# Optimization experiments

Measured on AMD Instinct MI355X. Metric: run time of the kernel, lower is better.

Reference implementation:

```python
import jax, jax.numpy as jnp
import numpy as np

B, S, H = 2, 2048, 2048
NH, NKV, HD = 16, 4, 128
SCALING = HD ** -0.5


def rotate_half(x):
    x1, x2 = jnp.split(x, 2, axis=-1)
    return jnp.concatenate((-x2, x1), axis=-1)


def apply_rope(t, cos, sin):
    # t: [B, nh, S, HD]; cos/sin: [B, S, HD] -> unsqueeze head dim
    c = cos[:, None, :, :]
    s = sin[:, None, :, :]
    return t * c + rotate_half(t) * s


def setup_inputs() -> dict:
    key = jax.random.key(0)
    k1, k2, k3, k4, k5 = jax.random.split(key, 5)
    hidden_states = jax.random.normal(k1, (B, S, H), dtype=jnp.float32)
    # real RoPE tables
    inv_freq = 1.0 / (10000.0 ** (jnp.arange(0, HD, 2, dtype=jnp.float32) / HD))
    pos = jnp.arange(S, dtype=jnp.float32)
    freqs = jnp.einsum('s,d->sd', pos, inv_freq)              # [S, HD/2]
    emb = jnp.concatenate((freqs, freqs), axis=-1)            # [S, HD]
    cos = jnp.broadcast_to(jnp.cos(emb)[None], (B, S, HD))
    sin = jnp.broadcast_to(jnp.sin(emb)[None], (B, S, HD))
    # additive causal mask [B, 1, S, S]
    causal = jnp.triu(jnp.full((S, S), -1e9, dtype=jnp.float32), k=1)
    attention_mask = jnp.broadcast_to(causal[None, None], (B, 1, S, S))
    sc = 0.02
    wq = jax.random.normal(k2, (NH * HD, H), dtype=jnp.float32) * sc
    wk = jax.random.normal(k3, (NKV * HD, H), dtype=jnp.float32) * sc
    wv = jax.random.normal(k4, (NKV * HD, H), dtype=jnp.float32) * sc
    wo = jax.random.normal(k5, (H, NH * HD), dtype=jnp.float32) * sc
    return {"hidden_states": hidden_states, "cos": cos, "sin": sin,
            "attention_mask": attention_mask, "wq": wq, "wk": wk, "wv": wv, "wo": wo}


def reference(hidden_states, cos, sin, attention_mask, wq, wk, wv, wo):
    x = hidden_states
    # fused-style QKV projections (nn.Linear: x @ W.T), split heads -> [B, nh, S, HD]
    q = (x @ wq.T).reshape(B, S, NH, HD).transpose(0, 2, 1, 3)
    k = (x @ wk.T).reshape(B, S, NKV, HD).transpose(0, 2, 1, 3)
    v = (x @ wv.T).reshape(B, S, NKV, HD).transpose(0, 2, 1, 3)
    q = apply_rope(q, cos, sin)
    k = apply_rope(k, cos, sin)
    # GQA: repeat KV heads (repeat_kv)
    n_rep = NH // NKV
    k = jnp.repeat(k, n_rep, axis=1)
    v = jnp.repeat(v, n_rep, axis=1)
    scores = jnp.einsum('bhqd,bhkd->bhqk', q, k) * SCALING + attention_mask
    attn = jax.nn.softmax(scores.astype(jnp.float32), axis=-1).astype(q.dtype)
    out = jnp.einsum('bhqk,bhkd->bhqd', attn, v)
    out = out.transpose(0, 2, 1, 3).reshape(B, S, NH * HD)
    out = out @ wo.T
    return (out, attn)
```

## Files before the change

### kernel.cpp

```cpp
#include <hip/hip_runtime.h>
#include <cstdint>
#include <cstddef>

typedef __bf16 bf16;
typedef __attribute__((ext_vector_type(8))) __bf16 bf16x8;
typedef __attribute__((ext_vector_type(4))) __bf16 bf16x4;
typedef __attribute__((ext_vector_type(4))) float f32x4;

constexpr int B_ = 2, S_ = 2048, H_ = 2048, NH_ = 16, NKV_ = 4, HD_ = 128;
constexpr float SCALE_ = 0.08838834764831845f;

#define GLDS16(g, l)                                                        \
  __builtin_amdgcn_global_load_lds(                                         \
      (const __attribute__((address_space(1))) void*)(g),                   \
      (__attribute__((address_space(3))) void*)(l), 16, 0, 0)

#define VMCNT0 asm volatile("s_waitcnt vmcnt(0)" ::: "memory")
#define VMCNT4 asm volatile("s_waitcnt vmcnt(4)" ::: "memory")
#define VMCNT8 asm volatile("s_waitcnt vmcnt(8)" ::: "memory")
#define BAR __builtin_amdgcn_s_barrier()

__global__ void cvt_all(const float* __restrict__ hs, const float* __restrict__ wq,
                        const float* __restrict__ wk, const float* __restrict__ wv,
                        const float* __restrict__ wo, bf16* __restrict__ xb,
                        bf16* __restrict__ w3b, bf16* __restrict__ wob) {
  const int stride = gridDim.x * blockDim.x;
  for (int i = blockIdx.x * blockDim.x + threadIdx.x; i < 4718592; i += stride) {
    const float4* s; bf16x4* d; int j;
    if (i < 2097152)      { s = (const float4*)hs; d = (bf16x4*)xb;            j = i; }
    else if (i < 3145728) { s = (const float4*)wq; d = (bf16x4*)w3b;           j = i - 2097152; }
    else if (i < 3407872) { s = (const float4*)wk; d = (bf16x4*)w3b + 1048576; j = i - 3145728; }
    else if (i < 3670016) { s = (const float4*)wv; d = (bf16x4*)w3b + 1310720; j = i - 3407872; }
    else                  { s = (const float4*)wo; d = (bf16x4*)wob;           j = i - 3670016; }
    float4 v = s[j];
    bf16x4 o;
    o[0] = (bf16)v.x; o[1] = (bf16)v.y; o[2] = (bf16)v.z; o[3] = (bf16)v.w;
    d[j] = o;
  }
}

template <int EPI>
__global__ __launch_bounds__(256, 2) void gemm_bt(const bf16* __restrict__ A,
                                                  const bf16* __restrict__ Bm, int K,
                                                  bf16* __restrict__ qb, bf16* __restrict__ kb,
                                                  bf16* __restrict__ vtb, float* __restrict__ Cout) {
  __shared__ __align__(16) bf16 As[2][128 * 64];
  __shared__ __align__(16) bf16 Bs[2][128 * 64];
  const int tid = threadIdx.x;
  const int lane = tid & 63;
  const int wid = tid >> 6;
  const int fid = blockIdx.y * 32 + blockIdx.x;
  const int nwg = gridDim.y * 32;
  const int swz = (fid & 7) * (nwg >> 3) + (fid >> 3);
  const int m0 = (swz & 31) * 128;
  const int n0 = (swz >> 5) * 128;
  const int wm = (wid >> 1) * 64, wn = (wid & 1) * 64;
  const int r = lane & 15, g = lane >> 4;
  f32x4 acc[4][4] = {};

  auto STAGE = [&](int kt, int cc) {
#pragma unroll
    for (int i = 0; i < 4; ++i) {
      int cb = wid * 256 + i * 64;
      int c64 = cb + lane;
      int row = c64 >> 3, cs = (c64 & 7) ^ (row & 7);
      GLDS16(A + (size_t)(m0 + row) * K + kt + cs * 8, &As[cc][cb * 8]);
      GLDS16(Bm + (size_t)(n0 + row) * K + kt + cs * 8, &Bs[cc][cb * 8]);
    }
  };

  STAGE(0, 0);
  int c = 0;
#pragma unroll 1
  for (int kt = 0; kt < K; kt += 64) {
    if (kt + 64 < K) {
      STAGE(kt + 64, c ^ 1);
      VMCNT8;
    } else {
      VMCNT0;
    }
    BAR;
#pragma unroll
    for (int ks = 0; ks < 2; ++ks) {
      bf16x8 af[4], bfr[4];
#pragma unroll
      for (int fm = 0; fm < 4; ++fm)
        af[fm] = *(const bf16x8*)(&As[c][(wm + fm * 16 + r) * 64 + (((ks * 4 + g) ^ (r & 7)) << 3)]);
#pragma unroll
      for (int fn = 0; fn < 4; ++fn)
        bfr[fn] = *(const bf16x8*)(&Bs[c][(wn + fn * 16 + r) * 64 + (((ks * 4 + g) ^ (r & 7)) << 3)]);
#pragma unroll
      for (int fm = 0; fm < 4; ++fm)
#pragma unroll
        for (int fn = 0; fn < 4; ++fn)
          acc[fm][fn] = __builtin_amdgcn_mfma_f32_16x16x32_bf16(af[fm], bfr[fn], acc[fm][fn], 0, 0, 0);
    }
    BAR;
    c ^= 1;
  }

#pragma unroll
  for (int fm = 0; fm < 4; ++fm)
#pragma unroll
    for (int fn = 0; fn < 4; ++fn)
#pragma unroll
      for (int rr = 0; rr < 4; ++rr) {
        int mm = m0 + wm + fm * 16 + g * 4 + rr;
        int nn = n0 + wn + fn * 16 + r;
        float v = acc[fm][fn][rr];
        if (EPI == 1) {
          Cout[(size_t)mm * 2048 + nn] = v;
        } else {
          int b = mm >> 11, s = mm & (S_ - 1);
          int d = nn & 127;
          if (nn < 2048) {
            int hh = nn >> 7;
            qb[(((size_t)b * NH_ + hh) * S_ + s) * HD_ + d] = (bf16)v;
          } else if (nn < 2560) {
            int hh = (nn - 2048) >> 7;
            kb[(((size_t)b * NKV_ + hh) * S_ + s) * HD_ + d] = (bf16)v;
          } else {
            int hh = (nn - 2560) >> 7;
            vtb[(((size_t)b * NKV_ + hh) * HD_ + d) * S_ + s] = (bf16)v;
          }
        }
      }
}

__global__ void rope_kernel(bf16* __restrict__ qb, bf16* __restrict__ kb,
                            const float* __restrict__ cosp, const float* __restrict__ sinp) {
  const int NQ = B_ * NH_ * S_;
  const int NK = B_ * NKV_ * S_;
  const int tot = (NQ + NK) * 8;
  int t = blockIdx.x * blockDim.x + threadIdx.x;
  if (t >= tot) return;
  const int oct = t & 7, rid = t >> 3;
  bf16* base;
  int b, s;
  if (rid < NQ) {
    base = qb + (size_t)rid * HD_;
    s = rid & (S_ - 1);
    b = rid >> 15;
  } else {
    int r2 = rid - NQ;
    base = kb + (size_t)r2 * HD_;
    s = r2 & (S_ - 1);
    b = r2 >> 13;
  }
  const int d = oct * 8;
  const float* cp = cosp + ((size_t)b * S_ + s) * HD_ + d;
  const float* sp = sinp + ((size_t)b * S_ + s) * HD_ + d;
  float4 c0 = *(const float4*)cp, c1 = *(const float4*)(cp + 4);
  float4 s0 = *(const float4*)sp, s1 = *(const float4*)(sp + 4);
  float cc[8] = {c0.x, c0.y, c0.z, c0.w, c1.x, c1.y, c1.z, c1.w};
  float ss[8] = {s0.x, s0.y, s0.z, s0.w, s1.x, s1.y, s1.z, s1.w};
  bf16x8 x1 = *(const bf16x8*)(base + d);
  bf16x8 x2 = *(const bf16x8*)(base + d + 64);
  bf16x8 o1, o2;
#pragma unroll
  for (int i = 0; i < 8; ++i) {
    float a = (float)x1[i], bb = (float)x2[i];
    o1[i] = (bf16)(a * cc[i] - bb * ss[i]);
    o2[i] = (bf16)(bb * cc[i] + a * ss[i]);
  }
  *(bf16x8*)(base + d) = o1;
  *(bf16x8*)(base + d + 64) = o2;
}

__global__ __launch_bounds__(256, 2) void attn_kernel(const bf16* __restrict__ qb,
                                                      const bf16* __restrict__ kb,
                                                      const bf16* __restrict__ vtb,
                                                      bf16* __restrict__ aob,
                                                      float* __restrict__ attn_out) {
  __shared__ __align__(16) bf16 Ks[2][64 * 128];
  __shared__ __align__(16) bf16 Vs[2][128 * 64];
  __shared__ __align__(16) bf16 Ps[64 * 64];
  const int bid = (blockIdx.x & 7) * 64 + (blockIdx.x >> 3);
  const int p = bid & 15;
  const int h = (bid >> 4) & 15;
  const int b = bid >> 8;
  const int kh = h >> 2;
  const int tid = threadIdx.x, lane = tid & 63, wid = tid >> 6;
  const int r = lane & 15, g = lane >> 4;

  const bf16* kbase = kb + ((size_t)b * NKV_ + kh) * S_ * HD_;
  const bf16* vbase = vtb + ((size_t)b * NKV_ + kh) * (size_t)HD_ * S_;
  const size_t ahead = (size_t)(b * NH_ + h) * S_;

  auto stageK = [&](int kt, int cc) {
#pragma unroll
    for (int i = 0; i < 4; ++i) {
      int base = i * 256 + wid * 64;
      int idx = base + lane;
      int row = idx >> 4, ch = (idx & 15) ^ (row & 7);
      GLDS16(kbase + (size_t)(kt * 64 + row) * HD_ + ch * 8, &Ks[cc][base * 8]);
    }
  };
  auto stageV = [&](int kt, int cc) {
#pragma unroll
    for (int i = 0; i < 4; ++i) {
      int base = i * 256 + wid * 64;
      int idx = base + lane;
      int row = idx >> 3, ch = (idx & 7) ^ (row & 7);
      GLDS16(vbase + (size_t)row * S_ + kt * 64 + ch * 8, &Vs[cc][base * 8]);
    }
  };

  int zc = 0;

#pragma unroll 1
  for (int sbi = 0; sbi < 2; ++sbi) {
    const int qt = sbi ? 31 - p : p;
    const int q0 = qt * 64;
    const int nt = qt + 1;
    const bf16* qsrc = qb + ((size_t)(b * NH_ + h) * S_ + q0) * HD_;

    bf16x8 qreg[4];
#pragma unroll
    for (int ks = 0; ks < 4; ++ks)
      qreg[ks] = *(const bf16x8*)(qsrc + (wid * 16 + r) * HD_ + ks * 32 + g * 8);

    float lsum = 0.f;
    stageK(0, 0);
    VMCNT0; BAR;
    int c = 0;
#pragma unroll 1
    for (int kt = 0; kt < nt; ++kt) {
      if (kt + 1 < nt) stageK(kt + 1, c ^ 1);
      const bool dz = (zc <= 30);
      if (dz) {
        int qtz, ktz;
        if (zc < 31 - p) { qtz = p; ktz = p + 1 + zc; }
        else             { qtz = 31 - p; ktz = zc + 1; }
        float* zdst = attn_out + (ahead + qtz * 64) * S_ + ktz * 64;
        float4 z = {0.f, 0.f, 0.f, 0.f};
#pragma unroll
        for (int i = 0; i < 4; ++i) {
          int idx = i * 256 + tid;
          *(float4*)(zdst + (size_t)(idx >> 4) * S_ + (idx & 15) * 4) = z;
        }
        ++zc;
      }
      f32x4 sacc[4] = {};
      __builtin_amdgcn_s_setprio(1);
#pragma unroll
      for (int ks = 0; ks < 4; ++ks)
#pragma unroll
        for (int fn = 0; fn < 4; ++fn) {
          bf16x8 kk = *(const bf16x8*)(&Ks[c][(fn * 16 + r) * 128 + (((ks * 4 + g) ^ (r & 7)) << 3)]);
          sacc[fn] = __builtin_amdgcn_mfma_f32_16x16x32_bf16(kk, qreg[ks], sacc[fn], 0, 0, 0);
        }
      __builtin_amdgcn_s_setprio(0);
      float ts = 0.f;
      if (kt == nt - 1) {
#pragma unroll
        for (int fn = 0; fn < 4; ++fn)
#pragma unroll
          for (int rr = 0; rr < 4; ++rr) {
            bool msk = (fn * 16 + g * 4 + rr) > (wid * 16 + r);
            ts += msk ? 0.f : __expf(sacc[fn][rr] * SCALE_);
          }
      } else {
#pragma unroll
        for (int fn = 0; fn < 4; ++fn)
#pragma unroll
          for (int rr = 0; rr < 4; ++rr) ts += __expf(sacc[fn][rr] * SCALE_);
      }
      ts += __shfl_xor(ts, 16);
      ts += __shfl_xor(ts, 32);
      lsum += ts;
      if (dz) { VMCNT4; } else { VMCNT0; }
      BAR;
      c ^= 1;
    }
    const float rl = 1.0f / lsum;

    f32x4 oacc[8] = {};
    const size_t arow0 = (ahead + q0) * S_;
    stageK(0, 0);
    stageV(0, 0);
    VMCNT0; BAR;
    c = 0;
#pragma unroll 1
    for (int kt = 0; kt < nt; ++kt) {
      if (kt + 1 < nt) { stageK(kt + 1, c ^ 1); stageV(kt + 1, c ^ 1); }
      const int k0 = kt * 64;
      f32x4 sacc[4] = {};
      __builtin_amdgcn_s_setprio(1);
#pragma unroll
      for (int ks = 0; ks < 4; ++ks)
#pragma unroll
        for (int fn = 0; fn < 4; ++fn) {
          bf16x8 kk = *(const bf16x8*)(&Ks[c][(fn * 16 + r) * 128 + (((ks * 4 + g) ^ (r & 7)) << 3)]);
          sacc[fn] = __builtin_amdgcn_mfma_f32_16x16x32_bf16(kk, qreg[ks], sacc[fn], 0, 0, 0);
        }
      __builtin_amdgcn_s_setprio(0);
      const int prow = (wid * 16 + r) * 64;
      if (kt == nt - 1) {
#pragma unroll
        for (int fn = 0; fn < 4; ++fn) {
          bf16x4 pk;
#pragma unroll
          for (int rr = 0; rr < 4; ++rr) {
            bool msk = (fn * 16 + g * 4 + rr) > (wid * 16 + r);
            pk[rr] = (bf16)(msk ? 0.f : __expf(sacc[fn][rr] * SCALE_) * rl);
          }
          *(bf16x4*)(&Ps[prow + ((((fn << 1) | (g >> 1)) ^ (r & 7)) << 3) + ((g & 1) << 2)]) = pk;
        }
      } else {
#pragma unroll
        for (int fn = 0; fn < 4; ++fn) {
          bf16x4 pk;
#pragma unroll
          for (int rr = 0; rr < 4; ++rr)
            pk[rr] = (bf16)(__expf(sacc[fn][rr] * SCALE_) * rl);
          *(bf16x4*)(&Ps[prow + ((((fn << 1) | (g >> 1)) ^ (r & 7)) << 3) + ((g & 1) << 2)]) = pk;
        }
      }
      {
        const int trow = tid >> 2, tcb = (tid & 3) * 16;
        float* dst = attn_out + arow0 + (size_t)trow * S_ + k0 + tcb;
        int ch0 = (tid & 3) * 2;
        bf16x8 p0 = *(const bf16x8*)(&Ps[trow * 64 + ((ch0 ^ (trow & 7)) << 3)]);
        bf16x8 p1 = *(const bf16x8*)(&Ps[trow * 64 + (((ch0 + 1) ^ (trow & 7)) << 3)]);
        float4 o0 = {(float)p0[0], (float)p0[1], (float)p0[2], (float)p0[3]};
        float4 o1 = {(float)p0[4], (float)p0[5], (float)p0[6], (float)p0[7]};
        float4 o2 = {(float)p1[0], (float)p1[1], (float)p1[2], (float)p1[3]};
        float4 o3 = {(float)p1[4], (float)p1[5], (float)p1[6], (float)p1[7]};
        *(float4*)(dst) = o0;
        *(float4*)(dst + 4) = o1;
        *(float4*)(dst + 8) = o2;
        *(float4*)(dst + 12) = o3;
      }
      __builtin_amdgcn_s_setprio(1);
#pragma unroll
      for (int ks = 0; ks < 2; ++ks) {
        bf16x8 pa = *(const bf16x8*)(&Ps[prow + (((ks * 4 + g) ^ (r & 7)) << 3)]);
#pragma unroll
        for (int fn = 0; fn < 8; ++fn) {
          bf16x8 vv = *(const bf16x8*)(&Vs[c][(fn * 16 + r) * 64 + (((ks * 4 + g) ^ (r & 7)) << 3)]);
          oacc[fn] = __builtin_amdgcn_mfma_f32_16x16x32_bf16(pa, vv, oacc[fn], 0, 0, 0);
        }
      }
      __builtin_amdgcn_s_setprio(0);
      VMCNT4; BAR;
      c ^= 1;
    }

#pragma unroll
    for (int fn = 0; fn < 8; ++fn)
#pragma unroll
      for (int rr = 0; rr < 4; ++rr) {
        int q = q0 + wid * 16 + g * 4 + rr;
        aob[((size_t)b * S_ + q) * 2048 + h * HD_ + fn * 16 + r] = (bf16)oacc[fn][rr];
      }
  }
}

extern "C" void kernel_launch(void* const* d_in, const int* in_sizes, int n_in,
                              void* d_out, int out_size, void* d_ws, size_t ws_size,
                              hipStream_t stream) {
  const float* hidden = (const float*)d_in[0];
  const float* cosp = (const float*)d_in[1];
  const float* sinp = (const float*)d_in[2];
  const float* wq = (const float*)d_in[4];
  const float* wk = (const float*)d_in[5];
  const float* wv = (const float*)d_in[6];
  const float* wo = (const float*)d_in[7];
  float* out = (float*)d_out;
  float* attn = out + (size_t)B_ * S_ * H_;

  char* ws = (char*)d_ws;
  bf16* xb  = (bf16*)(ws);
  bf16* w3b = (bf16*)(ws + (16ull << 20));
  bf16* wob = (bf16*)(ws + (28ull << 20));
  bf16* qb  = (bf16*)(ws + (36ull << 20));
  bf16* kb  = (bf16*)(ws + (52ull << 20));
  bf16* vtb = (bf16*)(ws + (56ull << 20));
  bf16* aob = (bf16*)(ws + (60ull << 20));

  cvt_all<<<2048, 256, 0, stream>>>(hidden, wq, wk, wv, wo, xb, w3b, wob);
  gemm_bt<0><<<dim3(32, 24), 256, 0, stream>>>(xb, w3b, 2048, qb, kb, vtb, nullptr);
  rope_kernel<<<2560, 256, 0, stream>>>(qb, kb, cosp, sinp);
  attn_kernel<<<512, 256, 0, stream>>>(qb, kb, vtb, aob, attn);
  gemm_bt<1><<<dim3(32, 16), 256, 0, stream>>>(aob, wob, 2048, nullptr, nullptr, nullptr, out);
}
```

Baseline: 349.7 us.

## Split attention into one q-tile per block, load V to registers, write probs directly

The attention kernel now gives each block a single query tile, in descending order, instead of a balanced pair of tiles. The grid doubles to 1024 blocks and the launch bound rises to 3 blocks per SM. V tiles are read straight from global memory into registers instead of being staged through LDS, which removes the Vs buffers and cuts shared memory use. Probabilities are written to attn_out directly from the fp32 softmax values rather than read back from LDS, and the zeroing of masked tiles is reorganised per block. These changes trade away the original load balancing and add VGPR pressure in exchange for more occupancy and less LDS traffic.

Result: slower. 449.1 us (+28.4%).

```diff
diff --git a/kernel.cpp b/kernel.cpp
--- a/kernel.cpp
+++ b/kernel.cpp
@@ -18,6 +18,7 @@
 #define VMCNT0 asm volatile("s_waitcnt vmcnt(0)" ::: "memory")
 #define VMCNT4 asm volatile("s_waitcnt vmcnt(4)" ::: "memory")
 #define VMCNT8 asm volatile("s_waitcnt vmcnt(8)" ::: "memory")
+#define VMCNT20 asm volatile("s_waitcnt vmcnt(20)" ::: "memory")
 #define BAR __builtin_amdgcn_s_barrier()
 
 __global__ void cvt_all(const float* __restrict__ hs, const float* __restrict__ wq,
@@ -167,25 +168,28 @@
   *(bf16x8*)(base + d + 64) = o2;
 }
 
-__global__ __launch_bounds__(256, 2) void attn_kernel(const bf16* __restrict__ qb,
+__global__ __launch_bounds__(256, 3) void attn_kernel(const bf16* __restrict__ qb,
                                                       const bf16* __restrict__ kb,
                                                       const bf16* __restrict__ vtb,
                                                       bf16* __restrict__ aob,
                                                       float* __restrict__ attn_out) {
   __shared__ __align__(16) bf16 Ks[2][64 * 128];
-  __shared__ __align__(16) bf16 Vs[2][128 * 64];
   __shared__ __align__(16) bf16 Ps[64 * 64];
-  const int bid = (blockIdx.x & 7) * 64 + (blockIdx.x >> 3);
-  const int p = bid & 15;
-  const int h = (bid >> 4) & 15;
-  const int b = bid >> 8;
+  const int bid = (blockIdx.x & 7) * 128 + (blockIdx.x >> 3);
+  const int qt = 31 - (bid & 31);
+  const int h = (bid >> 5) & 15;
+  const int b = bid >> 9;
   const int kh = h >> 2;
+  const int q0 = qt * 64;
+  const int nt = qt + 1;
   const int tid = threadIdx.x, lane = tid & 63, wid = tid >> 6;
   const int r = lane & 15, g = lane >> 4;
 
   const bf16* kbase = kb + ((size_t)b * NKV_ + kh) * S_ * HD_;
   const bf16* vbase = vtb + ((size_t)b * NKV_ + kh) * (size_t)HD_ * S_;
   const size_t ahead = (size_t)(b * NH_ + h) * S_;
+  const size_t arow0 = (ahead + q0) * S_;
+  const bf16* qsrc = qb + (ahead + q0) * HD_;
 
   auto stageK = [&](int kt, int cc) {
 #pragma unroll
@@ -196,164 +200,137 @@
       GLDS16(kbase + (size_t)(kt * 64 + row) * HD_ + ch * 8, &Ks[cc][base * 8]);
     }
   };
-  auto stageV = [&](int kt, int cc) {
+
+  bf16x8 qreg[4];
+#pragma unroll
+  for (int ks = 0; ks < 4; ++ks)
+    qreg[ks] = *(const bf16x8*)(qsrc + (wid * 16 + r) * HD_ + ks * 32 + g * 8);
+
+  float lsum = 0.f;
+  stageK(0, 0);
+  VMCNT0; BAR;
+  int c = 0;
+#pragma unroll 1
+  for (int kt = 0; kt < nt; ++kt) {
+    if (kt + 1 < nt) stageK(kt + 1, c ^ 1);
+    const int ktz = qt + 1 + kt;
+    const bool dz = (ktz <= 31);
+    if (dz) {
+      float* zdst = attn_out + arow0 + ktz * 64;
+      float4 z = {0.f, 0.f, 0.f, 0.f};
+#pragma unroll
+      for (int i = 0; i < 4; ++i) {
+        int idx = i * 256 + tid;
+        *(float4*)(zdst + (size_t)(idx >> 4) * S_ + (idx & 15) * 4) = z;
+      }
+    }
+    f32x4 sacc[4] = {};
+    __builtin_amdgcn_s_setprio(1);
+#pragma unroll
+    for (int ks = 0; ks < 4; ++ks)
+#pragma unroll
+      for (int fn = 0; fn < 4; ++fn) {
+        bf16x8 kk = *(const bf16x8*)(&Ks[c][(fn * 16 + r) * 128 + (((ks * 4 + g) ^ (r & 7)) << 3)]);
+        sacc[fn] = __builtin_amdgcn_mfma_f32_16x16x32_bf16(kk, qreg[ks], sacc[fn], 0, 0, 0);
+      }
+    __builtin_amdgcn_s_setprio(0);
+    float ts = 0.f;
+    if (kt == nt - 1) {
+#pragma unroll
+      for (int fn = 0; fn < 4; ++fn)
+#pragma unroll
+        for (int rr = 0; rr < 4; ++rr) {
+          bool msk = (fn * 16 + g * 4 + rr) > (wid * 16 + r);
+          ts += msk ? 0.f : __expf(sacc[fn][rr] * SCALE_);
+        }
+    } else {
+#pragma unroll
+      for (int fn = 0; fn < 4; ++fn)
+#pragma unroll
+        for (int rr = 0; rr < 4; ++rr) ts += __expf(sacc[fn][rr] * SCALE_);
+    }
+    ts += __shfl_xor(ts, 16);
+    ts += __shfl_xor(ts, 32);
+    lsum += ts;
+    if (dz) { VMCNT4; } else { VMCNT0; }
+    BAR;
+    c ^= 1;
+  }
+  const float rl = 1.0f / lsum;
+
+  f32x4 oacc[8] = {};
+  stageK(0, 0);
+  VMCNT0; BAR;
+  c = 0;
+#pragma unroll 1
+  for (int kt = 0; kt < nt; ++kt) {
+    const int k0 = kt * 64;
+    bf16x8 vv0[8], vv1[8];
+#pragma unroll
+    for (int fn = 0; fn < 8; ++fn)
+      vv0[fn] = *(const bf16x8*)(vbase + (size_t)(fn * 16 + r) * S_ + k0 + g * 8);
+#pragma unroll
+    for (int fn = 0; fn < 8; ++fn)
+      vv1[fn] = *(const bf16x8*)(vbase + (size_t)(fn * 16 + r) * S_ + k0 + 32 + g * 8);
+    if (kt + 1 < nt) stageK(kt + 1, c ^ 1);
+    VMCNT20;
+    BAR;
+    f32x4 sacc[4] = {};
+    __builtin_amdgcn_s_setprio(1);
+#pragma unroll
+    for (int ks = 0; ks < 4; ++ks)
+#pragma unroll
+      for (int fn = 0; fn < 4; ++fn) {
+        bf16x8 kk = *(const bf16x8*)(&Ks[c][(fn * 16 + r) * 128 + (((ks * 4 + g) ^ (r & 7)) << 3)]);
+        sacc[fn] = __builtin_amdgcn_mfma_f32_16x16x32_bf16(kk, qreg[ks], sacc[fn], 0, 0, 0);
+      }
+    __builtin_amdgcn_s_setprio(0);
+    const int prow = (wid * 16 + r) * 64;
+    const bool last = (kt == nt - 1);
+#pragma unroll
+    for (int fn = 0; fn < 4; ++fn) {
+      float4 pv4;
+      bf16x4 pk;
+#pragma unroll
+      for (int rr = 0; rr < 4; ++rr) {
+        bool msk = last && ((fn * 16 + g * 4 + rr) > (wid * 16 + r));
+        float f = msk ? 0.f : __expf(sacc[fn][rr] * SCALE_) * rl;
+        ((float*)&pv4)[rr] = f;
+        pk[rr] = (bf16)f;
+      }
+      *(float4*)(attn_out + arow0 + (size_t)(wid * 16 + r) * S_ + k0 + fn * 16 + g * 4) = pv4;
+      *(bf16x4*)(&Ps[prow + ((((fn << 1) | (g >> 1)) ^ (r & 7)) << 3) + ((g & 1) << 2)]) = pk;
+    }
+    __builtin_amdgcn_s_setprio(1);
+#pragma unroll
+    for (int ks = 0; ks < 2; ++ks) {
+      bf16x8 pa = *(const bf16x8*)(&Ps[prow + (((ks * 4 + g) ^ (r & 7)) << 3)]);
+#pragma unroll
+      for (int fn = 0; fn < 8; ++fn)
+        oacc[fn] = __builtin_amdgcn_mfma_f32_16x16x32_bf16(pa, ks ? vv1[fn] : vv0[fn], oacc[fn], 0, 0, 0);
+    }
+    __builtin_amdgcn_s_setprio(0);
+    BAR;
+    c ^= 1;
+  }
+
+#pragma unroll
+  for (int fn = 0; fn < 8; ++fn)
+#pragma unroll
+    for (int rr = 0; rr < 4; ++rr) {
+      int q = q0 + wid * 16 + g * 4 + rr;
+      aob[((size_t)b * S_ + q) * 2048 + h * HD_ + fn * 16 + r] = (bf16)oacc[fn][rr];
+    }
+
+#pragma unroll 1
+  for (int kt2 = 2 * qt + 2; kt2 <= 31; ++kt2) {
+    float* zdst = attn_out + arow0 + kt2 * 64;
+    float4 z = {0.f, 0.f, 0.f, 0.f};
 #pragma unroll
     for (int i = 0; i < 4; ++i) {
-      int base = i * 256 + wid * 64;
-      int idx = base + lane;
-      int row = idx >> 3, ch = (idx & 7) ^ (row & 7);
-      GLDS16(vbase + (size_t)row * S_ + kt * 64 + ch * 8, &Vs[cc][base * 8]);
-    }
-  };
-
-  int zc = 0;
-
-#pragma unroll 1
-  for (int sbi = 0; sbi < 2; ++sbi) {
-    const int qt = sbi ? 31 - p : p;
-    const int q0 = qt * 64;
-    const int nt = qt + 1;
-    const bf16* qsrc = qb + ((size_t)(b * NH_ + h) * S_ + q0) * HD_;
-
-    bf16x8 qreg[4];
-#pragma unroll
-    for (int ks = 0; ks < 4; ++ks)
-      qreg[ks] = *(const bf16x8*)(qsrc + (wid * 16 + r) * HD_ + ks * 32 + g * 8);
-
-    float lsum = 0.f;
-    stageK(0, 0);
-    VMCNT0; BAR;
-    int c = 0;
-#pragma unroll 1
-    for (int kt = 0; kt < nt; ++kt) {
-      if (kt + 1 < nt) stageK(kt + 1, c ^ 1);
-      const bool dz = (zc <= 30);
-      if (dz) {
-        int qtz, ktz;
-        if (zc < 31 - p) { qtz = p; ktz = p + 1 + zc; }
-        else             { qtz = 31 - p; ktz = zc + 1; }
-        float* zdst = attn_out + (ahead + qtz * 64) * S_ + ktz * 64;
-        float4 z = {0.f, 0.f, 0.f, 0.f};
-#pragma unroll
-        for (int i = 0; i < 4; ++i) {
-          int idx = i * 256 + tid;
-          *(float4*)(zdst + (size_t)(idx >> 4) * S_ + (idx & 15) * 4) = z;
-        }
-        ++zc;
-      }
-      f32x4 sacc[4] = {};
-      __builtin_amdgcn_s_setprio(1);
-#pragma unroll
-      for (int ks = 0; ks < 4; ++ks)
-#pragma unroll
-        for (int fn = 0; fn < 4; ++fn) {
-          bf16x8 kk = *(const bf16x8*)(&Ks[c][(fn * 16 + r) * 128 + (((ks * 4 + g) ^ (r & 7)) << 3)]);
-          sacc[fn] = __builtin_amdgcn_mfma_f32_16x16x32_bf16(kk, qreg[ks], sacc[fn], 0, 0, 0);
-        }
-      __builtin_amdgcn_s_setprio(0);
-      float ts = 0.f;
-      if (kt == nt - 1) {
-#pragma unroll
-        for (int fn = 0; fn < 4; ++fn)
-#pragma unroll
-          for (int rr = 0; rr < 4; ++rr) {
-            bool msk = (fn * 16 + g * 4 + rr) > (wid * 16 + r);
-            ts += msk ? 0.f : __expf(sacc[fn][rr] * SCALE_);
-          }
-      } else {
-#pragma unroll
-        for (int fn = 0; fn < 4; ++fn)
-#pragma unroll
-          for (int rr = 0; rr < 4; ++rr) ts += __expf(sacc[fn][rr] * SCALE_);
-      }
-      ts += __shfl_xor(ts, 16);
-      ts += __shfl_xor(ts, 32);
-      lsum += ts;
-      if (dz) { VMCNT4; } else { VMCNT0; }
-      BAR;
-      c ^= 1;
-    }
-    const float rl = 1.0f / lsum;
-
-    f32x4 oacc[8] = {};
-    const size_t arow0 = (ahead + q0) * S_;
-    stageK(0, 0);
-    stageV(0, 0);
-    VMCNT0; BAR;
-    c = 0;
-#pragma unroll 1
-    for (int kt = 0; kt < nt; ++kt) {
-      if (kt + 1 < nt) { stageK(kt + 1, c ^ 1); stageV(kt + 1, c ^ 1); }
-      const int k0 = kt * 64;
-      f32x4 sacc[4] = {};
-      __builtin_amdgcn_s_setprio(1);
-#pragma unroll
-      for (int ks = 0; ks < 4; ++ks)
-#pragma unroll
-        for (int fn = 0; fn < 4; ++fn) {
-          bf16x8 kk = *(const bf16x8*)(&Ks[c][(fn * 16 + r) * 128 + (((ks * 4 + g) ^ (r & 7)) << 3)]);
-          sacc[fn] = __builtin_amdgcn_mfma_f32_16x16x32_bf16(kk, qreg[ks], sacc[fn], 0, 0, 0);
-        }
-      __builtin_amdgcn_s_setprio(0);
-      const int prow = (wid * 16 + r) * 64;
-      if (kt == nt - 1) {
-#pragma unroll
-        for (int fn = 0; fn < 4; ++fn) {
-          bf16x4 pk;
-#pragma unroll
-          for (int rr = 0; rr < 4; ++rr) {
-            bool msk = (fn * 16 + g * 4 + rr) > (wid * 16 + r);
-            pk[rr] = (bf16)(msk ? 0.f : __expf(sacc[fn][rr] * SCALE_) * rl);
-          }
-          *(bf16x4*)(&Ps[prow + ((((fn << 1) | (g >> 1)) ^ (r & 7)) << 3) + ((g & 1) << 2)]) = pk;
-        }
-      } else {
-#pragma unroll
-        for (int fn = 0; fn < 4; ++fn) {
-          bf16x4 pk;
-#pragma unroll
-          for (int rr = 0; rr < 4; ++rr)
-            pk[rr] = (bf16)(__expf(sacc[fn][rr] * SCALE_) * rl);
-          *(bf16x4*)(&Ps[prow + ((((fn << 1) | (g >> 1)) ^ (r & 7)) << 3) + ((g & 1) << 2)]) = pk;
-        }
-      }
-      {
-        const int trow = tid >> 2, tcb = (tid & 3) * 16;
-        float* dst = attn_out + arow0 + (size_t)trow * S_ + k0 + tcb;
-        int ch0 = (tid & 3) * 2;
-        bf16x8 p0 = *(const bf16x8*)(&Ps[trow * 64 + ((ch0 ^ (trow & 7)) << 3)]);
-        bf16x8 p1 = *(const bf16x8*)(&Ps[trow * 64 + (((ch0 + 1) ^ (trow & 7)) << 3)]);
-        float4 o0 = {(float)p0[0], (float)p0[1], (float)p0[2], (float)p0[3]};
-        float4 o1 = {(float)p0[4], (float)p0[5], (float)p0[6], (float)p0[7]};
-        float4 o2 = {(float)p1[0], (float)p1[1], (float)p1[2], (float)p1[3]};
-        float4 o3 = {(float)p1[4], (float)p1[5], (float)p1[6], (float)p1[7]};
-        *(float4*)(dst) = o0;
-        *(float4*)(dst + 4) = o1;
-        *(float4*)(dst + 8) = o2;
-        *(float4*)(dst + 12) = o3;
-      }
-      __builtin_amdgcn_s_setprio(1);
-#pragma unroll
-      for (int ks = 0; ks < 2; ++ks) {
-        bf16x8 pa = *(const bf16x8*)(&Ps[prow + (((ks * 4 + g) ^ (r & 7)) << 3)]);
-#pragma unroll
-        for (int fn = 0; fn < 8; ++fn) {
-          bf16x8 vv = *(const bf16x8*)(&Vs[c][(fn * 16 + r) * 64 + (((ks * 4 + g) ^ (r & 7)) << 3)]);
-          oacc[fn] = __builtin_amdgcn_mfma_f32_16x16x32_bf16(pa, vv, oacc[fn], 0, 0, 0);
-        }
-      }
-      __builtin_amdgcn_s_setprio(0);
-      VMCNT4; BAR;
-      c ^= 1;
-    }
-
-#pragma unroll
-    for (int fn = 0; fn < 8; ++fn)
-#pragma unroll
-      for (int rr = 0; rr < 4; ++rr) {
-        int q = q0 + wid * 16 + g * 4 + rr;
-        aob[((size_t)b * S_ + q) * 2048 + h * HD_ + fn * 16 + r] = (bf16)oacc[fn][rr];
-      }
+      int idx = i * 256 + tid;
+      *(float4*)(zdst + (size_t)(idx >> 4) * S_ + (idx & 15) * 4) = z;
+    }
   }
 }
 
@@ -382,6 +359,6 @@
   cvt_all<<<2048, 256, 0, stream>>>(hidden, wq, wk, wv, wo, xb, w3b, wob);
   gemm_bt<0><<<dim3(32, 24), 256, 0, stream>>>(xb, w3b, 2048, qb, kb, vtb, nullptr);
   rope_kernel<<<2560, 256, 0, stream>>>(qb, kb, cosp, sinp);
-  attn_kernel<<<512, 256, 0, stream>>>(qb, kb, vtb, aob, attn);
+  attn_kernel<<<1024, 256, 0, stream>>>(qb, kb, vtb, aob, attn);
   gemm_bt<1><<<dim3(32, 16), 256, 0, stream>>>(aob, wob, 2048, nullptr, nullptr, nullptr, out);
 }
```
